# Kernel optimization log

Measured on AMD Instinct MI355X. Metric: run time of the kernel, lower is better.

Reference implementation:

```python
import jax, jax.numpy as jnp
import numpy as np

B, L, M, D = 8, 2048, 2048, 256


def setup_inputs() -> dict:
    key = jax.random.key(0)
    k1, k2, k3, k4, k5 = jax.random.split(key, 5)
    inp = jax.random.normal(k1, (B, L, D), dtype=jnp.float32)
    mem = jax.random.normal(k2, (B, M, D), dtype=jnp.float32)
    mask = jnp.ones((B, M), dtype=jnp.float32)
    # Learned parameters (Linear(D, 1, bias=False) -> weight vector of shape [D])
    w_input = jax.random.normal(k3, (D,), dtype=jnp.float32) / np.sqrt(D)
    w_memory = jax.random.normal(k4, (D,), dtype=jnp.float32) / np.sqrt(D)
    dot_scale = jax.random.uniform(k5, (D,), dtype=jnp.float32, minval=0.0, maxval=1.0 / np.sqrt(D))
    return {"input": inp, "memory": mem, "mask": mask,
            "w_input": w_input, "w_memory": w_memory, "dot_scale": dot_scale}


def reference(input, memory, mask, w_input, w_memory, dot_scale):
    # dropout with p=0.0 / eval mode -> identity
    input_dot = jnp.einsum('bld,d->bl', input, w_input)[:, :, None]      # [B, L, 1]
    memory_dot = jnp.einsum('bmd,d->bm', memory, w_memory)[:, None, :]   # [B, 1, M]
    cross_dot = jnp.einsum('bld,bmd->blm', input * dot_scale, memory)    # [B, L, M]
    att = input_dot + memory_dot + cross_dot                             # [B, L, M]
    att = att - 1e30 * (1.0 - mask[:, None, :])
    weight_one = jax.nn.softmax(att, axis=-1)                            # [B, L, M]
    output_one = jnp.einsum('blm,bmd->bld', weight_one, memory)          # [B, L, D]
    weight_two = jax.nn.softmax(jnp.max(att, axis=-1), axis=-1)[:, None, :]  # [B, 1, L]
    output_two = jnp.einsum('bol,bld->bod', weight_two, input)           # [B, 1, D]
    return jnp.concatenate(
        [input, output_one, input * output_one, output_two * output_one], axis=-1)
```

## Files before the change

### kernel.cpp

```cpp
#include <hip/hip_runtime.h>
#include <hip/hip_bf16.h>


typedef __bf16 bf16_t;
typedef bf16_t bf16x8 __attribute__((ext_vector_type(8)));
typedef bf16_t bf16x4 __attribute__((ext_vector_type(4)));
typedef float  f32x4  __attribute__((ext_vector_type(4)));

#define NB 8
#define NL 2048
#define NM 2048
#define ND 256
#define OUTW 1024
#define MT 32
#define MH 1024

__global__ __launch_bounds__(256) void dots_kernel(
    const float* __restrict__ input, const float* __restrict__ memory,
    const float* __restrict__ mask, const float* __restrict__ w_input,
    const float* __restrict__ w_memory,
    float* __restrict__ ws_idot, float* __restrict__ ws_mbias)
{
    int gid  = blockIdx.x * 4 + (threadIdx.x >> 6);
    int lane = threadIdx.x & 63;
    bool is_mem = gid >= NB * NL;
    int row = is_mem ? gid - NB * NL : gid;
    const float* src = (is_mem ? memory : input) + (size_t)row * ND + lane * 4;
    const float* w   = (is_mem ? w_memory : w_input) + lane * 4;
    float4 v = *(const float4*)src;
    float4 wv = *(const float4*)w;
    float s = v.x * wv.x + v.y * wv.y + v.z * wv.z + v.w * wv.w;
    #pragma unroll
    for (int off = 1; off < 64; off <<= 1) s += __shfl_xor(s, off, 64);
    if (lane == 0) {
        if (is_mem) ws_mbias[row] = s - 1e30f * (1.0f - mask[row]);
        else        ws_idot[row]  = s;
    }
}

__global__ __launch_bounds__(256, 2) void flash_kernel(
    const float* __restrict__ input, const float* __restrict__ memory,
    const float* __restrict__ dot_scale, const float* __restrict__ ws_mbias,
    float* __restrict__ out, float* __restrict__ ws_l, float* __restrict__ ws_m)
{
    int bid  = blockIdx.x;
    int half = bid & 1;
    int b    = (bid >> 1) & 7;
    int lt   = bid >> 4;
    int l0   = lt * 64;
    int m_base = half * MH;

    int t    = threadIdx.x;
    int wave = t >> 6;
    int lane = t & 63;
    int c    = lane & 15;
    int quad = lane >> 4;

    __shared__ __align__(16) bf16_t mem_lds[32 * 264];
    __shared__ __align__(16) bf16_t memT[ND * 40];
    __shared__ __align__(16) bf16_t p_lds[4 * 16 * 40];

    const float* qrow = input + (size_t)(b * NL + l0 + wave * 16 + c) * ND;
    bf16x8 qf[8];
    #pragma unroll
    for (int ks = 0; ks < 8; ++ks) {
        int d0 = ks * 32 + quad * 8;
        float4 a0 = *(const float4*)(qrow + d0);
        float4 a1 = *(const float4*)(qrow + d0 + 4);
        float4 s0 = *(const float4*)(dot_scale + d0);
        float4 s1 = *(const float4*)(dot_scale + d0 + 4);
        qf[ks][0] = (bf16_t)(a0.x * s0.x); qf[ks][1] = (bf16_t)(a0.y * s0.y);
        qf[ks][2] = (bf16_t)(a0.z * s0.z); qf[ks][3] = (bf16_t)(a0.w * s0.w);
        qf[ks][4] = (bf16_t)(a1.x * s1.x); qf[ks][5] = (bf16_t)(a1.y * s1.y);
        qf[ks][6] = (bf16_t)(a1.z * s1.z); qf[ks][7] = (bf16_t)(a1.w * s1.w);
    }

    bf16x8 ones;
    #pragma unroll
    for (int j = 0; j < 8; ++j) ones[j] = (bf16_t)1.0f;

    f32x4 oacc[16];
    #pragma unroll
    for (int i = 0; i < 16; ++i) oacc[i] = (f32x4){0.f, 0.f, 0.f, 0.f};
    f32x4 lacc = (f32x4){0.f, 0.f, 0.f, 0.f};
    float mpart[4] = {-3e38f, -3e38f, -3e38f, -3e38f};

    const float* memb    = memory + (size_t)b * NM * ND;
    const float* mbias_b = ws_mbias + b * NM + m_base;

    for (int it = 0; it < MH / MT; ++it) {
        int m0 = m_base + it * MT;
        __syncthreads();
        {
            int row = t >> 3, sub = t & 7;
            const float* src = memb + (size_t)(m0 + row) * ND;
            #pragma unroll
            for (int i = 0; i < 8; ++i) {
                int d = i * 32 + sub * 4;
                float4 v = *(const float4*)(src + d);
                bf16x4 w;
                w[0] = (bf16_t)v.x; w[1] = (bf16_t)v.y;
                w[2] = (bf16_t)v.z; w[3] = (bf16_t)v.w;
                *(bf16x4*)(&mem_lds[row * 264 + d]) = w;
            }
        }
        {
            const float* src = memb + (size_t)m0 * ND + t;
            #pragma unroll
            for (int i8 = 0; i8 < 4; ++i8) {
                bf16x8 w;
                #pragma unroll
                for (int j = 0; j < 8; ++j)
                    w[j] = (bf16_t)src[(size_t)(i8 * 8 + j) * ND];
                *(bf16x8*)(&memT[t * 40 + i8 * 8]) = w;
            }
        }
        __syncthreads();

        f32x4 s0 = (f32x4){0.f, 0.f, 0.f, 0.f};
        f32x4 s1 = (f32x4){0.f, 0.f, 0.f, 0.f};
        #pragma unroll
        for (int ks = 0; ks < 8; ++ks) {
            bf16x8 b0 = *(const bf16x8*)(&mem_lds[c * 264 + ks * 32 + quad * 8]);
            bf16x8 b1 = *(const bf16x8*)(&mem_lds[(16 + c) * 264 + ks * 32 + quad * 8]);
            s0 = __builtin_amdgcn_mfma_f32_16x16x32_bf16(qf[ks], b0, s0, 0, 0, 0);
            s1 = __builtin_amdgcn_mfma_f32_16x16x32_bf16(qf[ks], b1, s1, 0, 0, 0);
        }
        float mb0 = mbias_b[it * MT + c];
        float mb1 = mbias_b[it * MT + 16 + c];

        bf16_t* pw = &p_lds[wave * 16 * 40];
        #pragma unroll
        for (int r = 0; r < 4; ++r) {
            float v0 = s0[r] + mb0, v1 = s1[r] + mb1;
            mpart[r] = fmaxf(mpart[r], fmaxf(v0, v1));
            pw[(quad * 4 + r) * 40 + c]      = (bf16_t)__expf(v0);
            pw[(quad * 4 + r) * 40 + 16 + c] = (bf16_t)__expf(v1);
        }
        asm volatile("s_waitcnt lgkmcnt(0)" ::: "memory");

        bf16x8 pa = *(const bf16x8*)(&pw[c * 40 + quad * 8]);
        lacc = __builtin_amdgcn_mfma_f32_16x16x32_bf16(pa, ones, lacc, 0, 0, 0);
        #pragma unroll
        for (int tt = 0; tt < 16; ++tt) {
            bf16x8 bv = *(const bf16x8*)(&memT[(tt * 16 + c) * 40 + quad * 8]);
            oacc[tt] = __builtin_amdgcn_mfma_f32_16x16x32_bf16(pa, bv, oacc[tt], 0, 0, 0);
        }
    }

    #pragma unroll
    for (int off = 1; off < 16; off <<= 1) {
        #pragma unroll
        for (int r = 0; r < 4; ++r)
            mpart[r] = fmaxf(mpart[r], __shfl_xor(mpart[r], off, 64));
    }
    if (c == 0) {
        #pragma unroll
        for (int r = 0; r < 4; ++r) {
            int row = b * NL + l0 + wave * 16 + quad * 4 + r;
            ws_l[half * (NB * NL) + row] = lacc[r];
            ws_m[half * (NB * NL) + row] = mpart[r];
        }
    }
    float* oseg = out + (size_t)(b * NL + l0 + wave * 16) * OUTW + ND * (1 + half);
    #pragma unroll
    for (int tt = 0; tt < 16; ++tt)
        #pragma unroll
        for (int r = 0; r < 4; ++r)
            oseg[(size_t)(quad * 4 + r) * OUTW + tt * 16 + c] = oacc[tt][r];
}

__global__ __launch_bounds__(256) void combine_kernel(
    float* __restrict__ out, const float* __restrict__ ws_l)
{
    size_t tid = (size_t)blockIdx.x * 256 + threadIdx.x;
    size_t e = tid * 4;
    size_t row = e >> 8;
    int d = (int)(e & 255);
    float inv = 1.0f / (ws_l[row] + ws_l[NB * NL + row]);
    float* po = out + row * OUTW;
    float4 a  = *(const float4*)(po + ND + d);
    float4 bb = *(const float4*)(po + 2 * ND + d);
    float4 r;
    r.x = (a.x + bb.x) * inv; r.y = (a.y + bb.y) * inv;
    r.z = (a.z + bb.z) * inv; r.w = (a.w + bb.w) * inv;
    *(float4*)(po + ND + d) = r;
}

__global__ __launch_bounds__(256) void w2_kernel(
    const float* __restrict__ ws_idot, const float* __restrict__ ws_m,
    float* __restrict__ ws_w2)
{
    int b = blockIdx.x, t = threadIdx.x;
    __shared__ float red[256];
    float vals[8];
    float mx = -3e38f;
    #pragma unroll
    for (int i = 0; i < 8; ++i) {
        int l = i * 256 + t;
        float v = ws_idot[b * NL + l] +
                  fmaxf(ws_m[b * NL + l], ws_m[NB * NL + b * NL + l]);
        vals[i] = v;
        mx = fmaxf(mx, v);
    }
    red[t] = mx; __syncthreads();
    for (int s = 128; s > 0; s >>= 1) {
        if (t < s) red[t] = fmaxf(red[t], red[t + s]);
        __syncthreads();
    }
    mx = red[0]; __syncthreads();
    float se = 0.f;
    #pragma unroll
    for (int i = 0; i < 8; ++i) { vals[i] = __expf(vals[i] - mx); se += vals[i]; }
    red[t] = se; __syncthreads();
    for (int s = 128; s > 0; s >>= 1) {
        if (t < s) red[t] += red[t + s];
        __syncthreads();
    }
    float inv = 1.0f / red[0];
    #pragma unroll
    for (int i = 0; i < 8; ++i) ws_w2[b * NL + i * 256 + t] = vals[i] * inv;
}

__global__ __launch_bounds__(256) void o2_kernel(
    const float* __restrict__ input, const float* __restrict__ ws_w2,
    float* __restrict__ ws_o2)
{
    int b = blockIdx.x >> 4, slice = blockIdx.x & 15, d = threadIdx.x;
    float acc = 0.f;
    for (int i = 0; i < 128; ++i) {
        int l = slice * 128 + i;
        acc += ws_w2[b * NL + l] * input[(size_t)(b * NL + l) * ND + d];
    }
    atomicAdd(&ws_o2[b * ND + d], acc);
}

__global__ __launch_bounds__(256) void assembly_kernel(
    const float* __restrict__ input, const float* __restrict__ ws_o2,
    float* __restrict__ out)
{
    size_t tid = (size_t)blockIdx.x * 256 + threadIdx.x;
    size_t row = tid >> 6;
    int d = (int)(tid & 63) * 4;
    int b = (int)(row >> 11);
    float4 in = *(const float4*)(input + row * ND + d);
    float* po = out + row * OUTW;
    float4 o1 = *(const float4*)(po + ND + d);
    float4 o2 = *(const float4*)(ws_o2 + b * ND + d);
    *(float4*)(po + d) = in;
    float4 q; q.x = in.x * o1.x; q.y = in.y * o1.y; q.z = in.z * o1.z; q.w = in.w * o1.w;
    *(float4*)(po + 2 * ND + d) = q;
    float4 r; r.x = o2.x * o1.x; r.y = o2.y * o1.y; r.z = o2.z * o1.z; r.w = o2.w * o1.w;
    *(float4*)(po + 3 * ND + d) = r;
}

extern "C" void kernel_launch(void* const* d_in, const int* in_sizes, int n_in,
                              void* d_out, int out_size, void* d_ws, size_t ws_size,
                              hipStream_t stream) {
    const float* input     = (const float*)d_in[0];
    const float* memory    = (const float*)d_in[1];
    const float* mask      = (const float*)d_in[2];
    const float* w_input   = (const float*)d_in[3];
    const float* w_memory  = (const float*)d_in[4];
    const float* dot_scale = (const float*)d_in[5];
    float* out = (float*)d_out;
    float* ws  = (float*)d_ws;

    float* ws_idot  = ws;
    float* ws_mbias = ws + 16384;
    float* ws_l     = ws + 32768;
    float* ws_m     = ws + 65536;
    float* ws_w2    = ws + 98304;
    float* ws_o2    = ws + 114688;

    dots_kernel<<<8192, 256, 0, stream>>>(input, memory, mask, w_input, w_memory,
                                          ws_idot, ws_mbias);
    flash_kernel<<<512, 256, 0, stream>>>(input, memory, dot_scale, ws_mbias,
                                          out, ws_l, ws_m);
    combine_kernel<<<4096, 256, 0, stream>>>(out, ws_l);
    w2_kernel<<<8, 256, 0, stream>>>(ws_idot, ws_m, ws_w2);
    hipMemsetAsync(ws_o2, 0, NB * ND * sizeof(float), stream);
    o2_kernel<<<128, 256, 0, stream>>>(input, ws_w2, ws_o2);
    assembly_kernel<<<4096, 256, 0, stream>>>(input, ws_o2, out);
}
```

Before: 208.8 us.

## Use 32x32 MFMA tiles, register-prefetched memory staging, and fold combine into assembly

The flash kernel moves from 16x16x32 to 32x32x16 MFMA and doubles the L tile to 128 rows and the M tile to 64. It prefetches the next memory tile into registers while the current one is computed, and builds the transposed bf16 copy from those registers instead of doing strided global reads. The combine kernel is removed and its normalisation is folded into the assembly kernel, which drops one full pass over the output. The o2 reduction is also vectorised. The cost is fewer blocks (256, one per CU), more register pressure and dynamic LDS.

```diff
diff --git a/kernel.cpp b/kernel.cpp
--- a/kernel.cpp
+++ b/kernel.cpp
@@ -3,17 +3,23 @@
 
 
 typedef __bf16 bf16_t;
+typedef bf16_t bf16x4 __attribute__((ext_vector_type(4)));
 typedef bf16_t bf16x8 __attribute__((ext_vector_type(8)));
-typedef bf16_t bf16x4 __attribute__((ext_vector_type(4)));
 typedef float  f32x4  __attribute__((ext_vector_type(4)));
+typedef float  f32x16 __attribute__((ext_vector_type(16)));
 
 #define NB 8
 #define NL 2048
 #define NM 2048
 #define ND 256
 #define OUTW 1024
-#define MT 32
+#define MT 64
 #define MH 1024
+#define NIT (MH / MT)
+#define LT 128
+#define SK 264
+#define ST 72
+#define LDS_BYTES (MT * SK * 2 + ND * ST * 2 + 4 * 32 * ST * 2)
 
 __global__ __launch_bounds__(256) void dots_kernel(
     const float* __restrict__ input, const float* __restrict__ memory,
@@ -38,33 +44,36 @@
     }
 }
 
-__global__ __launch_bounds__(256, 2) void flash_kernel(
+__global__ __launch_bounds__(256, 1) void flash_kernel(
     const float* __restrict__ input, const float* __restrict__ memory,
     const float* __restrict__ dot_scale, const float* __restrict__ ws_mbias,
     float* __restrict__ out, float* __restrict__ ws_l, float* __restrict__ ws_m)
 {
+    extern __shared__ __align__(16) char smem[];
+    bf16_t* mem_lds = (bf16_t*)smem;
+    bf16_t* memT    = mem_lds + MT * SK;
+    bf16_t* p_lds   = memT + ND * ST;
+
     int bid  = blockIdx.x;
     int half = bid & 1;
     int b    = (bid >> 1) & 7;
     int lt   = bid >> 4;
-    int l0   = lt * 64;
+    int l0   = lt * LT;
     int m_base = half * MH;
 
     int t    = threadIdx.x;
-    int wave = t >> 6;
+    int w    = t >> 6;
     int lane = t & 63;
-    int c    = lane & 15;
-    int quad = lane >> 4;
-
-    __shared__ __align__(16) bf16_t mem_lds[32 * 264];
-    __shared__ __align__(16) bf16_t memT[ND * 40];
-    __shared__ __align__(16) bf16_t p_lds[4 * 16 * 40];
-
-    const float* qrow = input + (size_t)(b * NL + l0 + wave * 16 + c) * ND;
-    bf16x8 qf[8];
-    #pragma unroll
-    for (int ks = 0; ks < 8; ++ks) {
-        int d0 = ks * 32 + quad * 8;
+    int c    = lane & 31;
+    int h    = lane >> 5;
+    int dgrp = t & 63;
+    int mgrp = t >> 6;
+
+    const float* qrow = input + (size_t)(b * NL + l0 + w * 32 + c) * ND;
+    bf16x8 qf[16];
+    #pragma unroll
+    for (int ks = 0; ks < 16; ++ks) {
+        int d0 = ks * 16 + h * 8;
         float4 a0 = *(const float4*)(qrow + d0);
         float4 a1 = *(const float4*)(qrow + d0 + 4);
         float4 s0 = *(const float4*)(dot_scale + d0);
@@ -74,117 +83,118 @@
         qf[ks][4] = (bf16_t)(a1.x * s1.x); qf[ks][5] = (bf16_t)(a1.y * s1.y);
         qf[ks][6] = (bf16_t)(a1.z * s1.z); qf[ks][7] = (bf16_t)(a1.w * s1.w);
     }
-
     bf16x8 ones;
     #pragma unroll
     for (int j = 0; j < 8; ++j) ones[j] = (bf16_t)1.0f;
 
-    f32x4 oacc[16];
-    #pragma unroll
-    for (int i = 0; i < 16; ++i) oacc[i] = (f32x4){0.f, 0.f, 0.f, 0.f};
-    f32x4 lacc = (f32x4){0.f, 0.f, 0.f, 0.f};
-    float mpart[4] = {-3e38f, -3e38f, -3e38f, -3e38f};
+    f32x16 oacc[8];
+    #pragma unroll
+    for (int i = 0; i < 8; ++i)
+        #pragma unroll
+        for (int r = 0; r < 16; ++r) oacc[i][r] = 0.f;
+    f32x16 lacc;
+    #pragma unroll
+    for (int r = 0; r < 16; ++r) lacc[r] = 0.f;
+    float mpart[16];
+    #pragma unroll
+    for (int r = 0; r < 16; ++r) mpart[r] = -3e38f;
 
     const float* memb    = memory + (size_t)b * NM * ND;
-    const float* mbias_b = ws_mbias + b * NM + m_base;
-
-    for (int it = 0; it < MH / MT; ++it) {
+    const float* mbias_b = ws_mbias + b * NM;
+    bf16_t* pw = p_lds + w * 32 * ST;
+
+    float4 pf[16];
+    {
+        const float* src = memb + (size_t)(m_base + mgrp * 16) * ND + dgrp * 4;
+        #pragma unroll
+        for (int i = 0; i < 16; ++i) pf[i] = *(const float4*)(src + (size_t)i * ND);
+    }
+
+    #pragma unroll 1
+    for (int it = 0; it < NIT; ++it) {
         int m0 = m_base + it * MT;
         __syncthreads();
-        {
-            int row = t >> 3, sub = t & 7;
-            const float* src = memb + (size_t)(m0 + row) * ND;
+        #pragma unroll
+        for (int i = 0; i < 16; ++i) {
+            bf16x4 v;
+            v[0] = (bf16_t)pf[i].x; v[1] = (bf16_t)pf[i].y;
+            v[2] = (bf16_t)pf[i].z; v[3] = (bf16_t)pf[i].w;
+            *(bf16x4*)(&mem_lds[(mgrp * 16 + i) * SK + dgrp * 4]) = v;
+        }
+        #pragma unroll
+        for (int ddr = 0; ddr < 4; ++ddr) {
+            int dd = (ddr + dgrp) & 3;
+            bf16x8 lo, hi;
             #pragma unroll
             for (int i = 0; i < 8; ++i) {
-                int d = i * 32 + sub * 4;
-                float4 v = *(const float4*)(src + d);
-                bf16x4 w;
-                w[0] = (bf16_t)v.x; w[1] = (bf16_t)v.y;
-                w[2] = (bf16_t)v.z; w[3] = (bf16_t)v.w;
-                *(bf16x4*)(&mem_lds[row * 264 + d]) = w;
+                lo[i] = (bf16_t)((const float*)&pf[i])[dd];
+                hi[i] = (bf16_t)((const float*)&pf[8 + i])[dd];
             }
-        }
-        {
-            const float* src = memb + (size_t)m0 * ND + t;
+            bf16_t* dst = &memT[(dgrp * 4 + dd) * ST + mgrp * 16];
+            *(bf16x8*)dst = lo;
+            *(bf16x8*)(dst + 8) = hi;
+        }
+        __syncthreads();
+        if (it + 1 < NIT) {
+            const float* src = memb + (size_t)(m0 + MT + mgrp * 16) * ND + dgrp * 4;
             #pragma unroll
-            for (int i8 = 0; i8 < 4; ++i8) {
-                bf16x8 w;
-                #pragma unroll
-                for (int j = 0; j < 8; ++j)
-                    w[j] = (bf16_t)src[(size_t)(i8 * 8 + j) * ND];
-                *(bf16x8*)(&memT[t * 40 + i8 * 8]) = w;
+            for (int i = 0; i < 16; ++i) pf[i] = *(const float4*)(src + (size_t)i * ND);
+        }
+        f32x16 S0, S1;
+        #pragma unroll
+        for (int r = 0; r < 16; ++r) { S0[r] = 0.f; S1[r] = 0.f; }
+        #pragma unroll
+        for (int ks = 0; ks < 16; ++ks) {
+            bf16x8 b0 = *(const bf16x8*)(&mem_lds[c * SK + ks * 16 + h * 8]);
+            bf16x8 b1 = *(const bf16x8*)(&mem_lds[(32 + c) * SK + ks * 16 + h * 8]);
+            S0 = __builtin_amdgcn_mfma_f32_32x32x16_bf16(qf[ks], b0, S0, 0, 0, 0);
+            S1 = __builtin_amdgcn_mfma_f32_32x32x16_bf16(qf[ks], b1, S1, 0, 0, 0);
+        }
+        float mb0 = mbias_b[m0 + c];
+        float mb1 = mbias_b[m0 + 32 + c];
+        #pragma unroll
+        for (int r = 0; r < 16; ++r) {
+            int row = (r & 3) + 8 * (r >> 2) + 4 * h;
+            float v0 = S0[r] + mb0, v1 = S1[r] + mb1;
+            mpart[r] = fmaxf(mpart[r], fmaxf(v0, v1));
+            pw[row * ST + c]      = (bf16_t)__expf(v0);
+            pw[row * ST + 32 + c] = (bf16_t)__expf(v1);
+        }
+        asm volatile("s_waitcnt lgkmcnt(0)" ::: "memory");
+        #pragma unroll
+        for (int ks = 0; ks < 4; ++ks) {
+            bf16x8 pa = *(const bf16x8*)(&pw[c * ST + ks * 16 + h * 8]);
+            lacc = __builtin_amdgcn_mfma_f32_32x32x16_bf16(pa, ones, lacc, 0, 0, 0);
+            #pragma unroll
+            for (int dt = 0; dt < 8; ++dt) {
+                bf16x8 bv = *(const bf16x8*)(&memT[(dt * 32 + c) * ST + ks * 16 + h * 8]);
+                oacc[dt] = __builtin_amdgcn_mfma_f32_32x32x16_bf16(pa, bv, oacc[dt], 0, 0, 0);
             }
         }
-        __syncthreads();
-
-        f32x4 s0 = (f32x4){0.f, 0.f, 0.f, 0.f};
-        f32x4 s1 = (f32x4){0.f, 0.f, 0.f, 0.f};
-        #pragma unroll
-        for (int ks = 0; ks < 8; ++ks) {
-            bf16x8 b0 = *(const bf16x8*)(&mem_lds[c * 264 + ks * 32 + quad * 8]);
-            bf16x8 b1 = *(const bf16x8*)(&mem_lds[(16 + c) * 264 + ks * 32 + quad * 8]);
-            s0 = __builtin_amdgcn_mfma_f32_16x16x32_bf16(qf[ks], b0, s0, 0, 0, 0);
-            s1 = __builtin_amdgcn_mfma_f32_16x16x32_bf16(qf[ks], b1, s1, 0, 0, 0);
-        }
-        float mb0 = mbias_b[it * MT + c];
-        float mb1 = mbias_b[it * MT + 16 + c];
-
-        bf16_t* pw = &p_lds[wave * 16 * 40];
-        #pragma unroll
-        for (int r = 0; r < 4; ++r) {
-            float v0 = s0[r] + mb0, v1 = s1[r] + mb1;
-            mpart[r] = fmaxf(mpart[r], fmaxf(v0, v1));
-            pw[(quad * 4 + r) * 40 + c]      = (bf16_t)__expf(v0);
-            pw[(quad * 4 + r) * 40 + 16 + c] = (bf16_t)__expf(v1);
-        }
-        asm volatile("s_waitcnt lgkmcnt(0)" ::: "memory");
-
-        bf16x8 pa = *(const bf16x8*)(&pw[c * 40 + quad * 8]);
-        lacc = __builtin_amdgcn_mfma_f32_16x16x32_bf16(pa, ones, lacc, 0, 0, 0);
-        #pragma unroll
-        for (int tt = 0; tt < 16; ++tt) {
-            bf16x8 bv = *(const bf16x8*)(&memT[(tt * 16 + c) * 40 + quad * 8]);
-            oacc[tt] = __builtin_amdgcn_mfma_f32_16x16x32_bf16(pa, bv, oacc[tt], 0, 0, 0);
-        }
-    }
-
-    #pragma unroll
-    for (int off = 1; off < 16; off <<= 1) {
-        #pragma unroll
-        for (int r = 0; r < 4; ++r)
+    }
+
+    #pragma unroll
+    for (int off = 1; off < 32; off <<= 1) {
+        #pragma unroll
+        for (int r = 0; r < 16; ++r)
             mpart[r] = fmaxf(mpart[r], __shfl_xor(mpart[r], off, 64));
     }
     if (c == 0) {
         #pragma unroll
-        for (int r = 0; r < 4; ++r) {
-            int row = b * NL + l0 + wave * 16 + quad * 4 + r;
+        for (int r = 0; r < 16; ++r) {
+            int row = b * NL + l0 + w * 32 + (r & 3) + 8 * (r >> 2) + 4 * h;
             ws_l[half * (NB * NL) + row] = lacc[r];
             ws_m[half * (NB * NL) + row] = mpart[r];
         }
     }
-    float* oseg = out + (size_t)(b * NL + l0 + wave * 16) * OUTW + ND * (1 + half);
-    #pragma unroll
-    for (int tt = 0; tt < 16; ++tt)
-        #pragma unroll
-        for (int r = 0; r < 4; ++r)
-            oseg[(size_t)(quad * 4 + r) * OUTW + tt * 16 + c] = oacc[tt][r];
-}
-
-__global__ __launch_bounds__(256) void combine_kernel(
-    float* __restrict__ out, const float* __restrict__ ws_l)
-{
-    size_t tid = (size_t)blockIdx.x * 256 + threadIdx.x;
-    size_t e = tid * 4;
-    size_t row = e >> 8;
-    int d = (int)(e & 255);
-    float inv = 1.0f / (ws_l[row] + ws_l[NB * NL + row]);
-    float* po = out + row * OUTW;
-    float4 a  = *(const float4*)(po + ND + d);
-    float4 bb = *(const float4*)(po + 2 * ND + d);
-    float4 r;
-    r.x = (a.x + bb.x) * inv; r.y = (a.y + bb.y) * inv;
-    r.z = (a.z + bb.z) * inv; r.w = (a.w + bb.w) * inv;
-    *(float4*)(po + ND + d) = r;
+    float* oseg = out + (size_t)(b * NL + l0 + w * 32) * OUTW + ND * (1 + half);
+    #pragma unroll
+    for (int dt = 0; dt < 8; ++dt)
+        #pragma unroll
+        for (int r = 0; r < 16; ++r) {
+            int row = (r & 3) + 8 * (r >> 2) + 4 * h;
+            oseg[(size_t)row * OUTW + dt * 32 + c] = oacc[dt][r];
+        }
 }
 
 __global__ __launch_bounds__(256) void w2_kernel(
@@ -226,31 +236,44 @@
     const float* __restrict__ input, const float* __restrict__ ws_w2,
     float* __restrict__ ws_o2)
 {
-    int b = blockIdx.x >> 4, slice = blockIdx.x & 15, d = threadIdx.x;
-    float acc = 0.f;
-    for (int i = 0; i < 128; ++i) {
-        int l = slice * 128 + i;
-        acc += ws_w2[b * NL + l] * input[(size_t)(b * NL + l) * ND + d];
-    }
-    atomicAdd(&ws_o2[b * ND + d], acc);
+    int b = blockIdx.x >> 5, slice = blockIdx.x & 31;
+    int dq = threadIdx.x & 63, lq = threadIdx.x >> 6;
+    float4 acc = {0.f, 0.f, 0.f, 0.f};
+    #pragma unroll
+    for (int i = 0; i < 16; ++i) {
+        int l = slice * 64 + lq * 16 + i;
+        float wgt = ws_w2[b * NL + l];
+        float4 v = *(const float4*)(input + (size_t)(b * NL + l) * ND + dq * 4);
+        acc.x += wgt * v.x; acc.y += wgt * v.y;
+        acc.z += wgt * v.z; acc.w += wgt * v.w;
+    }
+    float* dst = ws_o2 + b * ND + dq * 4;
+    atomicAdd(dst + 0, acc.x); atomicAdd(dst + 1, acc.y);
+    atomicAdd(dst + 2, acc.z); atomicAdd(dst + 3, acc.w);
 }
 
 __global__ __launch_bounds__(256) void assembly_kernel(
     const float* __restrict__ input, const float* __restrict__ ws_o2,
-    float* __restrict__ out)
+    const float* __restrict__ ws_l, float* __restrict__ out)
 {
     size_t tid = (size_t)blockIdx.x * 256 + threadIdx.x;
     size_t row = tid >> 6;
     int d = (int)(tid & 63) * 4;
     int b = (int)(row >> 11);
+    float inv = 1.0f / (ws_l[row] + ws_l[NB * NL + row]);
+    float* po = out + row * OUTW;
     float4 in = *(const float4*)(input + row * ND + d);
-    float* po = out + row * OUTW;
-    float4 o1 = *(const float4*)(po + ND + d);
-    float4 o2 = *(const float4*)(ws_o2 + b * ND + d);
+    float4 pa = *(const float4*)(po + ND + d);
+    float4 pb = *(const float4*)(po + 2 * ND + d);
+    float4 o1;
+    o1.x = (pa.x + pb.x) * inv; o1.y = (pa.y + pb.y) * inv;
+    o1.z = (pa.z + pb.z) * inv; o1.w = (pa.w + pb.w) * inv;
+    float4 o2v = *(const float4*)(ws_o2 + b * ND + d);
     *(float4*)(po + d) = in;
+    *(float4*)(po + ND + d) = o1;
     float4 q; q.x = in.x * o1.x; q.y = in.y * o1.y; q.z = in.z * o1.z; q.w = in.w * o1.w;
     *(float4*)(po + 2 * ND + d) = q;
-    float4 r; r.x = o2.x * o1.x; r.y = o2.y * o1.y; r.z = o2.z * o1.z; r.w = o2.w * o1.w;
+    float4 r; r.x = o2v.x * o1.x; r.y = o2v.y * o1.y; r.z = o2v.z * o1.z; r.w = o2v.w * o1.w;
     *(float4*)(po + 3 * ND + d) = r;
 }
 
@@ -275,11 +298,10 @@
 
     dots_kernel<<<8192, 256, 0, stream>>>(input, memory, mask, w_input, w_memory,
                                           ws_idot, ws_mbias);
-    flash_kernel<<<512, 256, 0, stream>>>(input, memory, dot_scale, ws_mbias,
-                                          out, ws_l, ws_m);
-    combine_kernel<<<4096, 256, 0, stream>>>(out, ws_l);
+    flash_kernel<<<256, 256, LDS_BYTES, stream>>>(input, memory, dot_scale,
+                                                  ws_mbias, out, ws_l, ws_m);
     w2_kernel<<<8, 256, 0, stream>>>(ws_idot, ws_m, ws_w2);
     hipMemsetAsync(ws_o2, 0, NB * ND * sizeof(float), stream);
-    o2_kernel<<<128, 256, 0, stream>>>(input, ws_w2, ws_o2);
-    assembly_kernel<<<4096, 256, 0, stream>>>(input, ws_o2, out);
-}
+    o2_kernel<<<256, 256, 0, stream>>>(input, ws_w2, ws_o2);
+    assembly_kernel<<<4096, 256, 0, stream>>>(input, ws_o2, ws_l, out);
+}
```

Result: slower. 321.0 us (+53.7%).
